# Kernel tuning notes

Measured on AMD Instinct MI355X. Metric: run time of the kernel, lower is better.

Reference implementation:

```python
import jax, jax.numpy as jnp
import numpy as np

NUM_EXPERTS = 64
TOP_K = 2
HIDDEN = 4096
BATCH, SEQ = 4, 4096


def setup_inputs() -> dict:
    key = jax.random.key(0)
    k1, k2 = jax.random.split(key)
    hidden_states = jax.random.normal(k1, (BATCH, SEQ, HIDDEN), dtype=jnp.float32)
    # nn.init.normal_(gate.weight, std=0.02); Linear weight shape [E, H]
    gate_w = jax.random.normal(k2, (NUM_EXPERTS, HIDDEN), dtype=jnp.float32) * 0.02
    return {"hidden_states": hidden_states, "gate_w": gate_w}


def reference(hidden_states, gate_w):
    b, s, h = hidden_states.shape
    num_tokens = b * s
    hidden_flat = hidden_states.reshape(num_tokens, h)            # [N, H]
    router_logits = jnp.einsum('nh,eh->ne', hidden_flat, gate_w)  # [N, E]
    routing_probs = jax.nn.softmax(router_logits, axis=-1)        # [N, E]
    topk_probs, topk_indices = jax.lax.top_k(routing_probs, TOP_K)  # [N, K]
    # normalize_weights=True
    topk_probs = topk_probs / (topk_probs.sum(axis=-1, keepdims=True) + 1e-8)
    # routing index computation (grouped-GEMM dispatch metadata)
    flat_experts = topk_indices.reshape(-1)                        # [N*K]
    gather_indices = jnp.argsort(flat_experts, stable=True)        # token_indices[sort_order] == sort_order
    expert_counts = jnp.zeros((NUM_EXPERTS,), dtype=jnp.int32).at[flat_experts].add(1)
    expert_offsets = jnp.cumsum(expert_counts, axis=0)             # [E]
    routing_weights = topk_probs.reshape(-1)                       # [N*K]
    # eval mode: aux_loss and z_loss are zero constants
    aux_loss = jnp.float32(0.0)
    z_loss = jnp.float32(0.0)
    return routing_weights, topk_indices, expert_offsets, gather_indices, aux_loss, z_loss
```

## Files before the change

kernel.cpp:

```cpp
#include <hip/hip_runtime.h>
#include <hip/hip_bf16.h>
#include <stdint.h>

constexpr int HID  = 4096;
constexpr int NE   = 64;
constexpr int NTOK = 16384;
constexpr int NB2  = 128;

typedef __attribute__((ext_vector_type(8))) short short8;
typedef __attribute__((ext_vector_type(4))) float f32x4;

union Frag { uint32_t u[4]; short8 s; uint4 q; };

__device__ inline uint32_t cvtpk_bf16(float a, float b) {
  uint32_t r;
  asm("v_cvt_pk_bf16_f32 %0, %1, %2" : "=v"(r) : "v"(a), "v"(b));
  return r;
}
__device__ inline float asf(uint32_t u) { union { uint32_t u; float f; } c; c.u = u; return c.f; }

__device__ inline void split8(float4 p, float4 q, Frag& hi, Frag& lo) {
  float x[8] = {p.x, p.y, p.z, p.w, q.x, q.y, q.z, q.w};
#pragma unroll
  for (int j = 0; j < 4; ++j) {
    uint32_t h = cvtpk_bf16(x[2*j], x[2*j+1]);
    hi.u[j] = h;
    float r0 = x[2*j]   - asf(h << 16);
    float r1 = x[2*j+1] - asf(h & 0xFFFF0000u);
    lo.u[j] = cvtpk_bf16(r0, r1);
  }
}

__global__ __launch_bounds__(256) void prep_gate_k(
    const float* __restrict__ gw, uint4* __restrict__ gP) {
  int gid = blockIdx.x * 256 + threadIdx.x;
  int c = gid >> 9;
  int r = gid & 511;
  int n = r >> 7;
  int part = (r >> 6) & 1;
  int l = r & 63;
  int e  = n * 16 + (l & 15);
  int k0 = c * 32 + (l >> 4) * 8;
  const float* src = gw + (size_t)e * HID + k0;
  float4 p = *(const float4*)src;
  float4 q = *(const float4*)(src + 4);
  Frag hi, lo;
  split8(p, q, hi, lo);
  gP[gid] = part ? lo.q : hi.q;
}

template <int S>
__global__ __launch_bounds__(256) void gemm_k(
    const float* __restrict__ hidden, const uint4* __restrict__ gP,
    float* __restrict__ partial) {
  constexpr int NCH = 128 / S;
  const int tid = threadIdx.x;
  const int w = tid >> 6, l = tid & 63;
  const int b = blockIdx.x;
  const int s  = b % S;
  const int tb = b / S;
  const int t0 = tb * 128 + w * 32;
  const int row = l & 15, kg = l >> 4;

  const float* aBase = hidden + (size_t)(t0 + row) * HID + s * (HID / S) + kg * 8;
  const int cG0 = s * NCH;

  f32x4 acc[2][4] = {};
  float4 aC[2][2]; uint4 bC[4][2];

  auto LOAD = [&](int c, float4 (&a)[2][2], uint4 (&bb)[4][2]) {
    const float* ap = aBase + c * 32;
#pragma unroll
    for (int mt = 0; mt < 2; ++mt) {
      const float* p = ap + (size_t)mt * 16 * HID;
      a[mt][0] = *(const float4*)p;
      a[mt][1] = *(const float4*)(p + 4);
    }
    const uint4* bp = gP + (size_t)(cG0 + c) * 512 + l;
#pragma unroll
    for (int nt = 0; nt < 4; ++nt) {
      bb[nt][0] = bp[(nt * 2 + 0) * 64];
      bb[nt][1] = bp[(nt * 2 + 1) * 64];
    }
  };
  auto COMP = [&](float4 (&a)[2][2], uint4 (&bb)[4][2]) {
    Frag ahi[2], alo[2];
#pragma unroll
    for (int mt = 0; mt < 2; ++mt) split8(a[mt][0], a[mt][1], ahi[mt], alo[mt]);
#pragma unroll
    for (int nt = 0; nt < 4; ++nt) {
      Frag bhi, blo; bhi.q = bb[nt][0]; blo.q = bb[nt][1];
#pragma unroll
      for (int mt = 0; mt < 2; ++mt) {
        acc[mt][nt] = __builtin_amdgcn_mfma_f32_16x16x32_bf16(ahi[mt].s, bhi.s, acc[mt][nt], 0, 0, 0);
        acc[mt][nt] = __builtin_amdgcn_mfma_f32_16x16x32_bf16(ahi[mt].s, blo.s, acc[mt][nt], 0, 0, 0);
        acc[mt][nt] = __builtin_amdgcn_mfma_f32_16x16x32_bf16(alo[mt].s, bhi.s, acc[mt][nt], 0, 0, 0);
      }
    }
  };

  LOAD(0, aC, bC);
#pragma unroll 8
  for (int c = 0; c < NCH - 1; ++c) {
    float4 aN[2][2]; uint4 bN[4][2];
    LOAD(c + 1, aN, bN);
    COMP(aC, bC);
#pragma unroll
    for (int mt = 0; mt < 2; ++mt) { aC[mt][0] = aN[mt][0]; aC[mt][1] = aN[mt][1]; }
#pragma unroll
    for (int nt = 0; nt < 4; ++nt) { bC[nt][0] = bN[nt][0]; bC[nt][1] = bN[nt][1]; }
  }
  COMP(aC, bC);

  float* pout = partial + (size_t)s * NTOK * 64;
#pragma unroll
  for (int mt = 0; mt < 2; ++mt)
#pragma unroll
    for (int r = 0; r < 4; ++r) {
      int t = t0 + mt * 16 + kg * 4 + r;
      float* dst = pout + (size_t)t * 64 + (l & 15);
#pragma unroll
      for (int nt = 0; nt < 4; ++nt) dst[nt * 16] = acc[mt][nt][r];
    }
}

template <int S>
__global__ __launch_bounds__(256) void reduce_router_k(
    const float* __restrict__ partial, float* __restrict__ out_w,
    float* __restrict__ out_idx, int* __restrict__ flatE) {
  const int tid = threadIdx.x;
  const int te = tid & 15, tt = tid >> 4;
  const int t0 = blockIdx.x * 32;

  float acc[2][4] = {{0.f,0.f,0.f,0.f},{0.f,0.f,0.f,0.f}};
#pragma unroll
  for (int i = 0; i < 2; ++i) {
    int t = t0 + 2 * tt + i;
#pragma unroll
    for (int s = 0; s < S; ++s) {
      float4 v = *(const float4*)(partial + ((size_t)s * NTOK + t) * 64 + 4 * te);
      acc[i][0] += v.x; acc[i][1] += v.y; acc[i][2] += v.z; acc[i][3] += v.w;
    }
  }

#pragma unroll
  for (int i = 0; i < 2; ++i) {
    float v1 = -3.0e38f, v2 = -3.0e38f;
    int e1 = 0, e2 = 0;
#pragma unroll
    for (int j = 0; j < 4; ++j) {
      float v = acc[i][j];
      int e = 4 * te + j;
      if (v > v1 || (v == v1 && e < e1)) { v2 = v1; e2 = e1; v1 = v; e1 = e; }
      else if (v > v2 || (v == v2 && e < e2)) { v2 = v; e2 = e; }
    }
#pragma unroll
    for (int m = 1; m <= 8; m <<= 1) {
      float ov1 = __shfl_xor(v1, m); int oe1 = __shfl_xor(e1, m);
      float ov2 = __shfl_xor(v2, m); int oe2 = __shfl_xor(e2, m);
      bool aFirst = (v1 > ov1) || (v1 == ov1 && e1 < oe1);
      float w1v = aFirst ? v1 : ov1;  int w1e = aFirst ? e1 : oe1;
      float c1  = aFirst ? ov1 : v1;  int c1e = aFirst ? oe1 : e1;
      float c2  = aFirst ? v2 : ov2;  int c2e = aFirst ? e2 : oe2;
      bool sset = (c2 > c1) || (c2 == c1 && c2e < c1e);
      v1 = w1v; e1 = w1e;
      v2 = sset ? c2 : c1; e2 = sset ? c2e : c1e;
    }
    float sum = 0.f;
#pragma unroll
    for (int j = 0; j < 4; ++j) sum += __expf(acc[i][j] - v1);
#pragma unroll
    for (int m = 1; m <= 8; m <<= 1) sum += __shfl_xor(sum, m);

    float p1 = 1.0f / sum;
    float p2 = __expf(v2 - v1) / sum;
    float inv = 1.0f / (p1 + p2 + 1e-8f);
    float w1 = p1 * inv, w2 = p2 * inv;

    if (te == 0) {
      int t = t0 + 2 * tt + i;
      out_w[2 * t]       = w1;
      out_w[2 * t + 1]   = w2;
      out_idx[2 * t]     = (float)e1;
      out_idx[2 * t + 1] = (float)e2;
      flatE[2 * t]       = e1;
      flatE[2 * t + 1]   = e2;
    }
  }
}

__global__ __launch_bounds__(256) void hist_rank_k(
    const int* __restrict__ flatE, int* __restrict__ blockCounts,
    int* __restrict__ rankInBlock) {
  __shared__ int waveCnt[4][64];
  const int tid = threadIdx.x, blk = blockIdx.x;
  const int i = blk * 256 + tid;
  const int key = flatE[i];
  const int lane = tid & 63, w = tid >> 6;
  const unsigned long long below = (1ull << lane) - 1ull;

  int rankWave = 0, cntMyLane = 0;
  for (int e = 0; e < 64; ++e) {
    unsigned long long m = __ballot(key == e);
    if (e == key)  rankWave  = __popcll(m & below);
    if (e == lane) cntMyLane = __popcll(m);
  }
  waveCnt[w][lane] = cntMyLane;
  __syncthreads();

  int pre = 0;
  for (int w2 = 0; w2 < w; ++w2) pre += waveCnt[w2][key];
  rankInBlock[i] = pre + rankWave;

  if (tid < 64) {
    int tot = waveCnt[0][tid] + waveCnt[1][tid] + waveCnt[2][tid] + waveCnt[3][tid];
    blockCounts[blk * 64 + tid] = tot;
  }
}

__global__ void offsets_k(const int* __restrict__ blockCounts,
                          int* __restrict__ offTable,
                          float* __restrict__ out_off,
                          float* __restrict__ out_losses) {
  const int e = threadIdx.x;
  int run = 0;
  for (int b = 0; b < NB2; ++b) {
    offTable[e * NB2 + b] = run;
    run += blockCounts[b * 64 + e];
  }
  const int total = run;
  int inc = total;
  for (int d = 1; d < 64; d <<= 1) {
    int v = __shfl_up(inc, d);
    if (e >= d) inc += v;
  }
  out_off[e] = (float)inc;
  const int base = inc - total;
  for (int b = 0; b < NB2; ++b) offTable[e * NB2 + b] += base;
  if (e == 0) { out_losses[0] = 0.f; out_losses[1] = 0.f; }
}

__global__ __launch_bounds__(256) void scatter_k(
    const int* __restrict__ flatE, const int* __restrict__ rankInBlock,
    const int* __restrict__ offTable, float* __restrict__ out_gather) {
  const int i = blockIdx.x * 256 + threadIdx.x;
  const int key = flatE[i];
  const int pos = offTable[key * NB2 + blockIdx.x] + rankInBlock[i];
  out_gather[pos] = (float)i;
}

extern "C" void kernel_launch(void* const* d_in, const int* in_sizes, int n_in,
                              void* d_out, int out_size, void* d_ws, size_t ws_size,
                              hipStream_t stream) {
  const float* hidden = (const float*)d_in[0];
  const float* gate   = (const float*)d_in[1];

  float* out        = (float*)d_out;
  float* out_w      = out;
  float* out_idx    = out + 32768;
  float* out_off    = out + 65536;
  float* out_gather = out + 65600;
  float* out_losses = out + 98368;

  uint4* gP          = (uint4*)d_ws;
  int*   flatE       = (int*)((char*)d_ws + (1u << 20));
  int*   blockCounts = flatE + 32768;
  int*   rankInBlock = blockCounts + 8192;
  int*   offTable    = rankInBlock + 32768;
  float* partial     = (float*)((char*)d_ws + (2u << 20));

  const size_t fixed = 2u << 20;
  const size_t perS  = (size_t)NTOK * 64 * 4;
  int S = 1;
  if      (ws_size >= fixed + 8 * perS) S = 8;
  else if (ws_size >= fixed + 4 * perS) S = 4;
  else if (ws_size >= fixed + 2 * perS) S = 2;

  prep_gate_k<<<256, 256, 0, stream>>>(gate, gP);
  switch (S) {
    case 8:
      gemm_k<8><<<(NTOK / 128) * 8, 256, 0, stream>>>(hidden, gP, partial);
      reduce_router_k<8><<<NTOK / 32, 256, 0, stream>>>(partial, out_w, out_idx, flatE);
      break;
    case 4:
      gemm_k<4><<<(NTOK / 128) * 4, 256, 0, stream>>>(hidden, gP, partial);
      reduce_router_k<4><<<NTOK / 32, 256, 0, stream>>>(partial, out_w, out_idx, flatE);
      break;
    case 2:
      gemm_k<2><<<(NTOK / 128) * 2, 256, 0, stream>>>(hidden, gP, partial);
      reduce_router_k<2><<<NTOK / 32, 256, 0, stream>>>(partial, out_w, out_idx, flatE);
      break;
    default:
      gemm_k<1><<<(NTOK / 128) * 1, 256, 0, stream>>>(hidden, gP, partial);
      reduce_router_k<1><<<NTOK / 32, 256, 0, stream>>>(partial, out_w, out_idx, flatE);
      break;
  }
  hist_rank_k<<<NB2, 256, 0, stream>>>(flatE, blockCounts, rankInBlock);
  offsets_k<<<1, 64, 0, stream>>>(blockCounts, offTable, out_off, out_losses);
  scatter_k<<<NB2, 256, 0, stream>>>(flatE, rankInBlock, offTable, out_gather);
}
```

Baseline: 399.7 us.

## Fuse split-K router GEMM with in-block LDS reduction and top-2 softmax

The GEMM now splits K across 8 waves inside a 512-thread block covering 32 tokens. Partial logits are reduced in shared memory and the softmax/top-2 is done in the same kernel, so the global partial buffer and the separate reduce kernel go away. The offsets kernel is parallelised over 256 threads with a transposed offTable layout, and scatter indexes it to match. The software prefetch double-buffering in the GEMM loop is dropped, which may expose more load latency.

```diff
diff --git a/kernel.cpp b/kernel.cpp
--- a/kernel.cpp
+++ b/kernel.cpp
@@ -3,7 +3,6 @@
 #include <stdint.h>
 
 constexpr int HID  = 4096;
-constexpr int NE   = 64;
 constexpr int NTOK = 16384;
 constexpr int NB2  = 128;
 
@@ -49,47 +48,43 @@
   gP[gid] = part ? lo.q : hi.q;
 }
 
-template <int S>
-__global__ __launch_bounds__(256) void gemm_k(
+__global__ __launch_bounds__(512) void gemm_fused_k(
     const float* __restrict__ hidden, const uint4* __restrict__ gP,
-    float* __restrict__ partial) {
-  constexpr int NCH = 128 / S;
+    float* __restrict__ out_w, float* __restrict__ out_idx,
+    int* __restrict__ flatE) {
+  __shared__ float sm[8][32][68];
+
   const int tid = threadIdx.x;
   const int w = tid >> 6, l = tid & 63;
-  const int b = blockIdx.x;
-  const int s  = b % S;
-  const int tb = b / S;
-  const int t0 = tb * 128 + w * 32;
+  const int t0 = blockIdx.x * 32;
   const int row = l & 15, kg = l >> 4;
 
-  const float* aBase = hidden + (size_t)(t0 + row) * HID + s * (HID / S) + kg * 8;
-  const int cG0 = s * NCH;
+  const float* aBase = hidden + (size_t)(t0 + row) * HID + w * 512 + kg * 8;
+  const int c0 = w * 16;
 
   f32x4 acc[2][4] = {};
-  float4 aC[2][2]; uint4 bC[4][2];
-
-  auto LOAD = [&](int c, float4 (&a)[2][2], uint4 (&bb)[4][2]) {
-    const float* ap = aBase + c * 32;
+
+  for (int cc = 0; cc < 16; ++cc) {
+    const float* ap = aBase + cc * 32;
+    float4 a[2][2]; uint4 b[4][2];
 #pragma unroll
     for (int mt = 0; mt < 2; ++mt) {
       const float* p = ap + (size_t)mt * 16 * HID;
       a[mt][0] = *(const float4*)p;
       a[mt][1] = *(const float4*)(p + 4);
     }
-    const uint4* bp = gP + (size_t)(cG0 + c) * 512 + l;
+    const uint4* bp = gP + (size_t)(c0 + cc) * 512 + l;
 #pragma unroll
     for (int nt = 0; nt < 4; ++nt) {
-      bb[nt][0] = bp[(nt * 2 + 0) * 64];
-      bb[nt][1] = bp[(nt * 2 + 1) * 64];
-    }
-  };
-  auto COMP = [&](float4 (&a)[2][2], uint4 (&bb)[4][2]) {
+      b[nt][0] = bp[(nt * 2 + 0) * 64];
+      b[nt][1] = bp[(nt * 2 + 1) * 64];
+    }
     Frag ahi[2], alo[2];
 #pragma unroll
     for (int mt = 0; mt < 2; ++mt) split8(a[mt][0], a[mt][1], ahi[mt], alo[mt]);
 #pragma unroll
     for (int nt = 0; nt < 4; ++nt) {
-      Frag bhi, blo; bhi.q = bb[nt][0]; blo.q = bb[nt][1];
+      Frag bhi, blo; bhi.q = b[nt][0]; blo.q = b[nt][1];
 #pragma unroll
       for (int mt = 0; mt < 2; ++mt) {
         acc[mt][nt] = __builtin_amdgcn_mfma_f32_16x16x32_bf16(ahi[mt].s, bhi.s, acc[mt][nt], 0, 0, 0);
@@ -97,95 +92,67 @@
         acc[mt][nt] = __builtin_amdgcn_mfma_f32_16x16x32_bf16(alo[mt].s, bhi.s, acc[mt][nt], 0, 0, 0);
       }
     }
-  };
-
-  LOAD(0, aC, bC);
-#pragma unroll 8
-  for (int c = 0; c < NCH - 1; ++c) {
-    float4 aN[2][2]; uint4 bN[4][2];
-    LOAD(c + 1, aN, bN);
-    COMP(aC, bC);
-#pragma unroll
-    for (int mt = 0; mt < 2; ++mt) { aC[mt][0] = aN[mt][0]; aC[mt][1] = aN[mt][1]; }
-#pragma unroll
-    for (int nt = 0; nt < 4; ++nt) { bC[nt][0] = bN[nt][0]; bC[nt][1] = bN[nt][1]; }
-  }
-  COMP(aC, bC);
-
-  float* pout = partial + (size_t)s * NTOK * 64;
+  }
+
 #pragma unroll
   for (int mt = 0; mt < 2; ++mt)
 #pragma unroll
     for (int r = 0; r < 4; ++r) {
-      int t = t0 + mt * 16 + kg * 4 + r;
-      float* dst = pout + (size_t)t * 64 + (l & 15);
-#pragma unroll
-      for (int nt = 0; nt < 4; ++nt) dst[nt * 16] = acc[mt][nt][r];
-    }
-}
-
-template <int S>
-__global__ __launch_bounds__(256) void reduce_router_k(
-    const float* __restrict__ partial, float* __restrict__ out_w,
-    float* __restrict__ out_idx, int* __restrict__ flatE) {
-  const int tid = threadIdx.x;
-  const int te = tid & 15, tt = tid >> 4;
-  const int t0 = blockIdx.x * 32;
-
-  float acc[2][4] = {{0.f,0.f,0.f,0.f},{0.f,0.f,0.f,0.f}};
-#pragma unroll
-  for (int i = 0; i < 2; ++i) {
-    int t = t0 + 2 * tt + i;
-#pragma unroll
-    for (int s = 0; s < S; ++s) {
-      float4 v = *(const float4*)(partial + ((size_t)s * NTOK + t) * 64 + 4 * te);
-      acc[i][0] += v.x; acc[i][1] += v.y; acc[i][2] += v.z; acc[i][3] += v.w;
-    }
-  }
-
-#pragma unroll
-  for (int i = 0; i < 2; ++i) {
-    float v1 = -3.0e38f, v2 = -3.0e38f;
-    int e1 = 0, e2 = 0;
-#pragma unroll
-    for (int j = 0; j < 4; ++j) {
-      float v = acc[i][j];
-      int e = 4 * te + j;
-      if (v > v1 || (v == v1 && e < e1)) { v2 = v1; e2 = e1; v1 = v; e1 = e; }
-      else if (v > v2 || (v == v2 && e < e2)) { v2 = v; e2 = e; }
-    }
-#pragma unroll
-    for (int m = 1; m <= 8; m <<= 1) {
-      float ov1 = __shfl_xor(v1, m); int oe1 = __shfl_xor(e1, m);
-      float ov2 = __shfl_xor(v2, m); int oe2 = __shfl_xor(e2, m);
-      bool aFirst = (v1 > ov1) || (v1 == ov1 && e1 < oe1);
-      float w1v = aFirst ? v1 : ov1;  int w1e = aFirst ? e1 : oe1;
-      float c1  = aFirst ? ov1 : v1;  int c1e = aFirst ? oe1 : e1;
-      float c2  = aFirst ? v2 : ov2;  int c2e = aFirst ? e2 : oe2;
-      bool sset = (c2 > c1) || (c2 == c1 && c2e < c1e);
-      v1 = w1v; e1 = w1e;
-      v2 = sset ? c2 : c1; e2 = sset ? c2e : c1e;
-    }
-    float sum = 0.f;
-#pragma unroll
-    for (int j = 0; j < 4; ++j) sum += __expf(acc[i][j] - v1);
-#pragma unroll
-    for (int m = 1; m <= 8; m <<= 1) sum += __shfl_xor(sum, m);
-
-    float p1 = 1.0f / sum;
-    float p2 = __expf(v2 - v1) / sum;
-    float inv = 1.0f / (p1 + p2 + 1e-8f);
-    float w1 = p1 * inv, w2 = p2 * inv;
-
-    if (te == 0) {
-      int t = t0 + 2 * tt + i;
-      out_w[2 * t]       = w1;
-      out_w[2 * t + 1]   = w2;
-      out_idx[2 * t]     = (float)e1;
-      out_idx[2 * t + 1] = (float)e2;
-      flatE[2 * t]       = e1;
-      flatE[2 * t + 1]   = e2;
-    }
+      int tl = mt * 16 + kg * 4 + r;
+#pragma unroll
+      for (int nt = 0; nt < 4; ++nt)
+        sm[w][tl][nt * 16 + row] = acc[mt][nt][r];
+    }
+  __syncthreads();
+
+  const int te = tid & 15, tl = tid >> 4;
+  float av[4] = {0.f, 0.f, 0.f, 0.f};
+#pragma unroll
+  for (int ww = 0; ww < 8; ++ww) {
+    float4 v = *(const float4*)&sm[ww][tl][4 * te];
+    av[0] += v.x; av[1] += v.y; av[2] += v.z; av[3] += v.w;
+  }
+
+  float v1 = -3.0e38f, v2 = -3.0e38f;
+  int e1 = 0, e2 = 0;
+#pragma unroll
+  for (int j = 0; j < 4; ++j) {
+    float v = av[j];
+    int e = 4 * te + j;
+    if (v > v1 || (v == v1 && e < e1)) { v2 = v1; e2 = e1; v1 = v; e1 = e; }
+    else if (v > v2 || (v == v2 && e < e2)) { v2 = v; e2 = e; }
+  }
+#pragma unroll
+  for (int m = 1; m <= 8; m <<= 1) {
+    float ov1 = __shfl_xor(v1, m); int oe1 = __shfl_xor(e1, m);
+    float ov2 = __shfl_xor(v2, m); int oe2 = __shfl_xor(e2, m);
+    bool aFirst = (v1 > ov1) || (v1 == ov1 && e1 < oe1);
+    float w1v = aFirst ? v1 : ov1;  int w1e = aFirst ? e1 : oe1;
+    float c1  = aFirst ? ov1 : v1;  int c1e = aFirst ? oe1 : e1;
+    float c2  = aFirst ? v2 : ov2;  int c2e = aFirst ? e2 : oe2;
+    bool sset = (c2 > c1) || (c2 == c1 && c2e < c1e);
+    v1 = w1v; e1 = w1e;
+    v2 = sset ? c2 : c1; e2 = sset ? c2e : c1e;
+  }
+  float sum = 0.f;
+#pragma unroll
+  for (int j = 0; j < 4; ++j) sum += __expf(av[j] - v1);
+#pragma unroll
+  for (int m = 1; m <= 8; m <<= 1) sum += __shfl_xor(sum, m);
+
+  float p1 = 1.0f / sum;
+  float p2 = __expf(v2 - v1) / sum;
+  float inv = 1.0f / (p1 + p2 + 1e-8f);
+  float w1 = p1 * inv, w2 = p2 * inv;
+
+  if (te == 0) {
+    int t = t0 + tl;
+    out_w[2 * t]       = w1;
+    out_w[2 * t + 1]   = w2;
+    out_idx[2 * t]     = (float)e1;
+    out_idx[2 * t + 1] = (float)e2;
+    flatE[2 * t]       = e1;
+    flatE[2 * t + 1]   = e2;
   }
 }
 
@@ -218,26 +185,38 @@
   }
 }
 
-__global__ void offsets_k(const int* __restrict__ blockCounts,
-                          int* __restrict__ offTable,
-                          float* __restrict__ out_off,
-                          float* __restrict__ out_losses) {
-  const int e = threadIdx.x;
-  int run = 0;
-  for (int b = 0; b < NB2; ++b) {
-    offTable[e * NB2 + b] = run;
+__global__ __launch_bounds__(256) void offsets_k(
+    const int* __restrict__ blockCounts, int* __restrict__ offTable,
+    float* __restrict__ out_off, float* __restrict__ out_losses) {
+  __shared__ int cnt[4][64];
+  __shared__ int baseLds[64];
+  const int tid = threadIdx.x;
+  const int e = tid & 63, q = tid >> 6;
+
+  int s = 0;
+  for (int b = q * 32; b < q * 32 + 32; ++b) s += blockCounts[b * 64 + e];
+  cnt[q][e] = s;
+  __syncthreads();
+
+  if (tid < 64) {
+    int tot = cnt[0][e] + cnt[1][e] + cnt[2][e] + cnt[3][e];
+    int inc = tot;
+    for (int d = 1; d < 64; d <<= 1) {
+      int v = __shfl_up(inc, d);
+      if (e >= d) inc += v;
+    }
+    out_off[e] = (float)inc;
+    baseLds[e] = inc - tot;
+    if (e == 0) { out_losses[0] = 0.f; out_losses[1] = 0.f; }
+  }
+  __syncthreads();
+
+  int run = baseLds[e];
+  for (int q2 = 0; q2 < q; ++q2) run += cnt[q2][e];
+  for (int b = q * 32; b < q * 32 + 32; ++b) {
+    offTable[b * 64 + e] = run;
     run += blockCounts[b * 64 + e];
   }
-  const int total = run;
-  int inc = total;
-  for (int d = 1; d < 64; d <<= 1) {
-    int v = __shfl_up(inc, d);
-    if (e >= d) inc += v;
-  }
-  out_off[e] = (float)inc;
-  const int base = inc - total;
-  for (int b = 0; b < NB2; ++b) offTable[e * NB2 + b] += base;
-  if (e == 0) { out_losses[0] = 0.f; out_losses[1] = 0.f; }
 }
 
 __global__ __launch_bounds__(256) void scatter_k(
@@ -245,7 +224,7 @@
     const int* __restrict__ offTable, float* __restrict__ out_gather) {
   const int i = blockIdx.x * 256 + threadIdx.x;
   const int key = flatE[i];
-  const int pos = offTable[key * NB2 + blockIdx.x] + rankInBlock[i];
+  const int pos = offTable[blockIdx.x * 64 + key] + rankInBlock[i];
   out_gather[pos] = (float)i;
 }
 
@@ -267,35 +246,10 @@
   int*   blockCounts = flatE + 32768;
   int*   rankInBlock = blockCounts + 8192;
   int*   offTable    = rankInBlock + 32768;
-  float* partial     = (float*)((char*)d_ws + (2u << 20));
-
-  const size_t fixed = 2u << 20;
-  const size_t perS  = (size_t)NTOK * 64 * 4;
-  int S = 1;
-  if      (ws_size >= fixed + 8 * perS) S = 8;
-  else if (ws_size >= fixed + 4 * perS) S = 4;
-  else if (ws_size >= fixed + 2 * perS) S = 2;
 
   prep_gate_k<<<256, 256, 0, stream>>>(gate, gP);
-  switch (S) {
-    case 8:
-      gemm_k<8><<<(NTOK / 128) * 8, 256, 0, stream>>>(hidden, gP, partial);
-      reduce_router_k<8><<<NTOK / 32, 256, 0, stream>>>(partial, out_w, out_idx, flatE);
-      break;
-    case 4:
-      gemm_k<4><<<(NTOK / 128) * 4, 256, 0, stream>>>(hidden, gP, partial);
-      reduce_router_k<4><<<NTOK / 32, 256, 0, stream>>>(partial, out_w, out_idx, flatE);
-      break;
-    case 2:
-      gemm_k<2><<<(NTOK / 128) * 2, 256, 0, stream>>>(hidden, gP, partial);
-      reduce_router_k<2><<<NTOK / 32, 256, 0, stream>>>(partial, out_w, out_idx, flatE);
-      break;
-    default:
-      gemm_k<1><<<(NTOK / 128) * 1, 256, 0, stream>>>(hidden, gP, partial);
-      reduce_router_k<1><<<NTOK / 32, 256, 0, stream>>>(partial, out_w, out_idx, flatE);
-      break;
-  }
+  gemm_fused_k<<<NTOK / 32, 512, 0, stream>>>(hidden, gP, out_w, out_idx, flatE);
   hist_rank_k<<<NB2, 256, 0, stream>>>(flatE, blockCounts, rankInBlock);
-  offsets_k<<<1, 64, 0, stream>>>(blockCounts, offTable, out_off, out_losses);
+  offsets_k<<<1, 256, 0, stream>>>(blockCounts, offTable, out_off, out_losses);
   scatter_k<<<NB2, 256, 0, stream>>>(flatE, rankInBlock, offTable, out_gather);
 }
```

New measurement: 378.2 us. 5.4% less time.
